# Kernel optimization log

Measured on AMD Instinct MI355X. Metric: run time of the kernel, lower is better.

Reference implementation:

```python
import jax, jax.numpy as jnp
import numpy as np

N = 100000      # nodes
E = 1600000     # edges
D_IN = 128      # input_dim
H = 256         # hidden_dim
L = 3           # num_layers
B = 64          # graphs per batch
BN_EPS = 1e-5


def setup_inputs() -> dict:
    key = jax.random.key(0)
    ks = jax.random.split(key, 8)
    x = jax.random.normal(ks[0], (N, D_IN), dtype=jnp.float32)
    edge_index = jax.random.randint(ks[1], (2, E), 0, N, dtype=jnp.int32)
    batch = jnp.sort(jax.random.randint(ks[2], (N,), 0, B, dtype=jnp.int32))
    W0 = jax.random.normal(ks[3], (D_IN, H), dtype=jnp.float32) / np.sqrt(D_IN)
    W_rest = jax.random.normal(ks[4], (L - 1, H, H), dtype=jnp.float32) / np.sqrt(H)
    b = jax.random.normal(ks[5], (L, H), dtype=jnp.float32) * 0.01
    gamma = 1.0 + jax.random.normal(ks[6], (L, H), dtype=jnp.float32) * 0.01
    beta = jax.random.normal(ks[7], (L, H), dtype=jnp.float32) * 0.01
    return {"x": x, "W0": W0, "W_rest": W_rest, "b": b, "gamma": gamma,
            "beta": beta, "edge_index": edge_index, "batch": batch}


def reference(x, W0, W_rest, b, gamma, beta, edge_index, batch):
    src, dst = edge_index[0], edge_index[1]
    # GCN symmetric normalization with self-loops: deg = in-degree + 1
    deg = jax.ops.segment_sum(jnp.ones((E,), x.dtype), dst, num_segments=N) + 1.0
    dis = jax.lax.rsqrt(deg)                   # deg^{-1/2}, [N]
    enorm = dis[src] * dis[dst]                # per-edge norm, [E]
    self_norm = (dis * dis)[:, None]           # self-loop norm = 1/deg, [N,1]

    def gcn_bn_relu(h, W, bb, g, be):
        h = h @ W                                                  # [N,H]
        agg = jax.ops.segment_sum(h[src] * enorm[:, None], dst, num_segments=N)
        h = agg + h * self_norm + bb                               # self-loop + bias
        # BatchNorm1d (training mode: batch stats, biased variance)
        m = h.mean(axis=0)
        v = h.var(axis=0)
        h = (h - m) * jax.lax.rsqrt(v + BN_EPS) * g + be
        return jax.nn.relu(h)                                      # dropout = identity (eval)

    h = gcn_bn_relu(x, W0, b[0], gamma[0], beta[0])
    for i in range(L - 1):
        h = gcn_bn_relu(h, W_rest[i], b[i + 1], gamma[i + 1], beta[i + 1])

    # segment pooling per graph (att_pool in the original is dead code: not returned)
    counts = jax.ops.segment_sum(jnp.ones((N,), h.dtype), batch, num_segments=B)
    mean_pool = jax.ops.segment_sum(h, batch, num_segments=B) / counts[:, None]
    max_pool = jax.ops.segment_max(h, batch, num_segments=B)
    return jnp.concatenate([mean_pool, max_pool], axis=1)          # [B, 2H]
```

## Files before the change

### kernel.cpp

```cpp
#include <hip/hip_runtime.h>
#include <hip/hip_bf16.h>
#include <stdint.h>


#define NN 100000
#define EE 1600000
#define BB 64
#define MPAD 100096

typedef __attribute__((ext_vector_type(8))) short short8;
typedef __attribute__((ext_vector_type(4))) float f32x4;

__device__ __forceinline__ float bflo(uint32_t v){ return __uint_as_float(v << 16); }
__device__ __forceinline__ float bfhi(uint32_t v){ return __uint_as_float(v & 0xffff0000u); }
__device__ __forceinline__ uint32_t bfrne(float x){
  uint32_t u = __float_as_uint(x);
  return (u + 0x7fffu + ((u >> 16) & 1u)) >> 16;
}
__device__ __forceinline__ uint32_t bfpack(float a, float b){ return bfrne(a) | (bfrne(b) << 16); }

__device__ __forceinline__ void gload_lds16(const void* g, void* l){
  __builtin_amdgcn_global_load_lds(
      (const __attribute__((address_space(1))) uint32_t*)g,
      (__attribute__((address_space(3))) uint32_t*)l, 16, 0, 0);
}

__global__ void k_deg(const int* __restrict__ dst, int* __restrict__ degi){
  for (int e = blockIdx.x * blockDim.x + threadIdx.x; e < EE; e += gridDim.x * blockDim.x)
    atomicAdd(&degi[dst[e]], 1);
}

__global__ void k_dis(const int* __restrict__ degi, float* __restrict__ dis){
  int n = blockIdx.x * 256 + threadIdx.x;
  if (n < NN) dis[n] = rsqrtf((float)degi[n] + 1.0f);
}

__global__ void k_scan1(const int* __restrict__ degi, int* __restrict__ rp, int* __restrict__ bsum){
  __shared__ int lds[256];
  int b = blockIdx.x, t = threadIdx.x;
  int base = b * 1024 + t * 4;
  int v0 = (base + 0 < NN) ? degi[base + 0] : 0;
  int v1 = (base + 1 < NN) ? degi[base + 1] : 0;
  int v2 = (base + 2 < NN) ? degi[base + 2] : 0;
  int v3 = (base + 3 < NN) ? degi[base + 3] : 0;
  int s = v0 + v1 + v2 + v3;
  lds[t] = s; __syncthreads();
  for (int off = 1; off < 256; off <<= 1){
    int x = (t >= off) ? lds[t - off] : 0; __syncthreads();
    lds[t] += x; __syncthreads();
  }
  int excl = lds[t] - s;
  if (t == 255) bsum[b] = lds[255];
  if (base + 0 < NN) rp[base + 0] = excl;
  if (base + 1 < NN) rp[base + 1] = excl + v0;
  if (base + 2 < NN) rp[base + 2] = excl + v0 + v1;
  if (base + 3 < NN) rp[base + 3] = excl + v0 + v1 + v2;
}

__global__ void k_scan2(int* __restrict__ bsum, int nb){
  if (blockIdx.x == 0 && threadIdx.x == 0){
    int run = 0;
    for (int i = 0; i < nb; ++i){ int t = bsum[i]; bsum[i] = run; run += t; }
  }
}

__global__ void k_scan3(int* __restrict__ rp, int* __restrict__ cursor, const int* __restrict__ bsum){
  int b = blockIdx.x, t = threadIdx.x;
  int add = bsum[b];
  int base = b * 1024 + t * 4;
  #pragma unroll
  for (int j = 0; j < 4; ++j){
    int i = base + j;
    if (i < NN){ int v = rp[i] + add; rp[i] = v; cursor[i] = v; }
  }
  if (b == 0 && t == 0) rp[NN] = EE;
}

__global__ void k_fill(const int* __restrict__ src, const int* __restrict__ dst,
                       const float* __restrict__ dis, int* __restrict__ cursor,
                       long long* __restrict__ cp){
  for (int e = blockIdx.x * blockDim.x + threadIdx.x; e < EE; e += gridDim.x * blockDim.x){
    int s = src[e], d = dst[e];
    int pos = atomicAdd(&cursor[d], 1);
    float nrm = dis[s] * dis[d];
    long long v = (long long)(unsigned int)s | ((long long)(unsigned int)__float_as_uint(nrm) << 32);
    cp[pos] = v;
  }
}

__global__ void k_wt(const float* __restrict__ W, uint16_t* __restrict__ Wt, int K){
  int i = blockIdx.x * 256 + threadIdx.x;
  if (i >= 256 * K) return;
  int c = i / K, k = i - c * K;
  Wt[i] = (uint16_t)bfrne(W[k * 256 + c]);
}

__global__ void k_cvtx(const float* __restrict__ x, uint32_t* __restrict__ Xb){
  int i = blockIdx.x * 256 + threadIdx.x;
  if (i >= MPAD * 64) return;
  int row = i >> 6;
  uint32_t r = 0u;
  if (row < NN){
    int col = (i & 63) * 2;
    r = bfpack(x[row * 128 + col], x[row * 128 + col + 1]);
  }
  Xb[i] = r;
}

template<int K>
__global__ void k_agg(const uint32_t* __restrict__ Xin, const int* __restrict__ rp,
                      const long long* __restrict__ cp, const float* __restrict__ dis,
                      uint32_t* __restrict__ Xout){
  constexpr int LPR = K / 2;
  constexpr int RPAR = 256 / LPR;
  constexpr int SEQ = 4;
  int lane = threadIdx.x & (LPR - 1);
  int slot = threadIdx.x / LPR;
  int row0 = blockIdx.x * (RPAR * SEQ);
  for (int rr = 0; rr < SEQ; ++rr){
    int row = row0 + rr * RPAR + slot;
    if (row >= MPAD) continue;
    if (row >= NN){ Xout[(size_t)row * LPR + lane] = 0u; continue; }
    int beg = rp[row], end = rp[row + 1];
    float a0 = 0.f, a1 = 0.f;
    int e = beg;
    for (; e + 8 <= end; e += 8){
      long long p[8];
      #pragma unroll
      for (int u = 0; u < 8; ++u) p[u] = cp[e + u];
      uint32_t v[8];
      #pragma unroll
      for (int u = 0; u < 8; ++u) v[u] = Xin[(size_t)(int)p[u] * LPR + lane];
      #pragma unroll
      for (int u = 0; u < 8; ++u){
        float w = __uint_as_float((uint32_t)((unsigned long long)p[u] >> 32));
        a0 += w * bflo(v[u]); a1 += w * bfhi(v[u]);
      }
    }
    for (; e < end; ++e){
      long long p0 = cp[e];
      int s = (int)p0; float w = __uint_as_float((uint32_t)((unsigned long long)p0 >> 32));
      uint32_t v = Xin[(size_t)s * LPR + lane];
      a0 += w * bflo(v); a1 += w * bfhi(v);
    }
    float dv = dis[row]; float sn = dv * dv;
    uint32_t vs = Xin[(size_t)row * LPR + lane];
    a0 += sn * bflo(vs); a1 += sn * bfhi(vs);
    Xout[(size_t)row * LPR + lane] = bfpack(a0, a1);
  }
}

template<int K>
__global__ __launch_bounds__(256) void k_gemm(const uint16_t* __restrict__ A,
                                              const uint16_t* __restrict__ Bt,
                                              uint32_t* __restrict__ Cb,
                                              float* __restrict__ gstat){
  __shared__ __align__(16) uint16_t lA[2][4096];
  __shared__ __align__(16) uint16_t lB[2][4096];
  __shared__ float lstat[256];
  int tid = threadIdx.x;
  int l = tid & 63;
  int bm = blockIdx.x, bn = blockIdx.y;
  lstat[tid] = 0.f;

  f32x4 acc[4][4];
  #pragma unroll
  for (int m = 0; m < 4; ++m)
    #pragma unroll
    for (int n = 0; n < 4; ++n){ f32x4 z = {0.f,0.f,0.f,0.f}; acc[m][n] = z; }

  int w = tid >> 6, wr = w >> 1, wc = w & 1;
  int rbase = wr * 64, cbase = wc * 64;
  int lrow = l & 15, lk8 = l >> 4;

  auto stage = [&](int kt, int buf){
    #pragma unroll
    for (int i = 0; i < 2; ++i){
      int c = i * 256 + tid;
      int k8 = c >> 7, r = c & 127;
      size_t ga = (size_t)(bm * 128 + r) * K + kt * 32 + k8 * 8;
      size_t gb = (size_t)(bn * 128 + r) * K + kt * 32 + k8 * 8;
      gload_lds16((const char*)(A + ga), (char*)&lA[buf][c * 8]);
      gload_lds16((const char*)(Bt + gb), (char*)&lB[buf][c * 8]);
    }
  };

  stage(0, 0);
  __syncthreads();
  constexpr int NT = K / 32;
  for (int kt = 0; kt < NT; ++kt){
    int cur = kt & 1;
    if (kt + 1 < NT) stage(kt + 1, cur ^ 1);
    short8 afr[4], bfr[4];
    #pragma unroll
    for (int m = 0; m < 4; ++m)
      afr[m] = *(const short8*)&lA[cur][(lk8 * 128 + rbase + m * 16 + lrow) * 8];
    #pragma unroll
    for (int n = 0; n < 4; ++n)
      bfr[n] = *(const short8*)&lB[cur][(lk8 * 128 + cbase + n * 16 + lrow) * 8];
    #pragma unroll
    for (int m = 0; m < 4; ++m)
      #pragma unroll
      for (int n = 0; n < 4; ++n)
        acc[m][n] = __builtin_amdgcn_mfma_f32_16x16x32_bf16(afr[m], bfr[n], acc[m][n], 0, 0, 0);
    __syncthreads();
  }

  int grow0 = bm * 128 + rbase + (l >> 4) * 4;
  int gcol0 = bn * 128 + cbase + (l & 15);
  uint16_t* C16 = (uint16_t*)Cb;
  float sa[4] = {0.f,0.f,0.f,0.f}, sb[4] = {0.f,0.f,0.f,0.f};
  #pragma unroll
  for (int m = 0; m < 4; ++m){
    #pragma unroll
    for (int n = 0; n < 4; ++n){
      int col = gcol0 + n * 16;
      int r0 = grow0 + m * 16;
      f32x4 v = acc[m][n];
      #pragma unroll
      for (int q = 0; q < 4; ++q){
        C16[(size_t)(r0 + q) * 256 + col] = (uint16_t)bfrne(v[q]);
        sa[n] += v[q]; sb[n] += v[q] * v[q];
      }
    }
  }
  #pragma unroll
  for (int n = 0; n < 4; ++n){
    int cl = wc * 64 + n * 16 + lrow;
    atomicAdd(&lstat[cl], sa[n]);
    atomicAdd(&lstat[128 + cl], sb[n]);
  }
  __syncthreads();
  float* rep = gstat + (size_t)(bm & 7) * 512;
  if (tid < 128){
    atomicAdd(&rep[bn * 128 + tid], lstat[tid]);
    atomicAdd(&rep[256 + bn * 128 + tid], lstat[128 + tid]);
  }
}

__global__ void k_finalize(const float* __restrict__ stats, const float* __restrict__ gamma,
                           const float* __restrict__ beta, float* __restrict__ ss){
  int c = threadIdx.x;
  float s = 0.f, s2 = 0.f;
  #pragma unroll
  for (int r = 0; r < 8; ++r){
    s  += stats[r * 512 + c];
    s2 += stats[r * 512 + 256 + c];
  }
  float mean = s / (float)NN;
  float var  = s2 / (float)NN - mean * mean;
  float rstd = rsqrtf(var + 1e-5f);
  float sc = gamma[c] * rstd;
  ss[c] = sc;
  ss[256 + c] = beta[c] - mean * sc;
}

__global__ void k_bnapply(const uint4* __restrict__ Y, const float* __restrict__ ss,
                          uint4* __restrict__ X){
  int i = blockIdx.x * 256 + threadIdx.x;
  if (i >= MPAD * 32) return;
  uint4 v = Y[i];
  int c0 = (i & 31) * 8;
  float r0 = fmaxf(bflo(v.x) * ss[c0 + 0] + ss[256 + c0 + 0], 0.f);
  float r1 = fmaxf(bfhi(v.x) * ss[c0 + 1] + ss[256 + c0 + 1], 0.f);
  float r2 = fmaxf(bflo(v.y) * ss[c0 + 2] + ss[256 + c0 + 2], 0.f);
  float r3 = fmaxf(bfhi(v.y) * ss[c0 + 3] + ss[256 + c0 + 3], 0.f);
  float r4 = fmaxf(bflo(v.z) * ss[c0 + 4] + ss[256 + c0 + 4], 0.f);
  float r5 = fmaxf(bfhi(v.z) * ss[c0 + 5] + ss[256 + c0 + 5], 0.f);
  float r6 = fmaxf(bflo(v.w) * ss[c0 + 6] + ss[256 + c0 + 6], 0.f);
  float r7 = fmaxf(bfhi(v.w) * ss[c0 + 7] + ss[256 + c0 + 7], 0.f);
  uint4 o;
  o.x = bfpack(r0, r1); o.y = bfpack(r2, r3);
  o.z = bfpack(r4, r5); o.w = bfpack(r6, r7);
  X[i] = o;
}

__global__ void k_segstart(const int* __restrict__ batch, int* __restrict__ seg){
  int g = threadIdx.x;
  if (g > BB) return;
  if (g == BB){ seg[BB] = NN; return; }
  int lo = 0, hi = NN;
  while (lo < hi){ int mid = (lo + hi) >> 1; if (batch[mid] < g) lo = mid + 1; else hi = mid; }
  seg[g] = lo;
}

__global__ void k_pool(const uint32_t* __restrict__ X, const int* __restrict__ seg,
                       float* __restrict__ out){
  int g = blockIdx.x, t = threadIdx.x;
  int s = seg[g], e = seg[g + 1];
  float sm0 = 0.f, sm1 = 0.f, mx0 = 0.f, mx1 = 0.f;
  #pragma unroll 4
  for (int r = s; r < e; ++r){
    uint32_t v = X[(size_t)r * 128 + t];
    float a = bflo(v), b2 = bfhi(v);
    sm0 += a; sm1 += b2;
    mx0 = fmaxf(mx0, a); mx1 = fmaxf(mx1, b2);
  }
  float inv = 1.0f / (float)(e - s);
  out[g * 512 + 2 * t] = sm0 * inv;
  out[g * 512 + 2 * t + 1] = sm1 * inv;
  out[g * 512 + 256 + 2 * t] = mx0;
  out[g * 512 + 256 + 2 * t + 1] = mx1;
}

extern "C" void kernel_launch(void* const* d_in, const int* in_sizes, int n_in,
                              void* d_out, int out_size, void* d_ws, size_t ws_size,
                              hipStream_t stream){
  const float* x     = (const float*)d_in[0];
  const float* W0    = (const float*)d_in[1];
  const float* Wr    = (const float*)d_in[2];
  const float* gamma = (const float*)d_in[4];
  const float* beta  = (const float*)d_in[5];
  const int*   ei    = (const int*)d_in[6];
  const int*   batch = (const int*)d_in[7];
  const int* esrc = ei;
  const int* edst = ei + EE;
  float* out = (float*)d_out;

  char* base = (char*)d_ws;
  size_t off = 0;
  auto alloc = [&](size_t b)->char*{
    char* p = base + off; off = (off + b + 255) & ~(size_t)255; return p;
  };
  uint32_t* Xbuf = (uint32_t*)alloc((size_t)MPAD * 256 * 2);
  uint32_t* Xagg = (uint32_t*)alloc((size_t)MPAD * 256 * 2);
  uint32_t* Y    = (uint32_t*)alloc((size_t)MPAD * 256 * 2);
  uint16_t* Wt0  = (uint16_t*)alloc(256 * 128 * 2);
  uint16_t* Wt1  = (uint16_t*)alloc(256 * 256 * 2);
  uint16_t* Wt2  = (uint16_t*)alloc(256 * 256 * 2);
  int*   degi   = (int*)  alloc((size_t)NN * 4);
  float* dis    = (float*)alloc((size_t)NN * 4);
  int*   rp     = (int*)  alloc((size_t)(NN + 1) * 4);
  int*   cursor = (int*)  alloc((size_t)NN * 4);
  int*   bsum   = (int*)  alloc(128 * 4);
  long long* cp = (long long*)alloc((size_t)EE * 8);
  float* stats  = (float*)alloc(8 * 512 * 4);
  float* ss     = (float*)alloc(512 * 4);
  int*   seg    = (int*)  alloc((BB + 1) * 4);

  hipMemsetAsync(degi, 0, (size_t)NN * 4, stream);
  k_deg<<<2048, 256, 0, stream>>>(edst, degi);
  k_dis<<<391, 256, 0, stream>>>(degi, dis);
  k_scan1<<<98, 256, 0, stream>>>(degi, rp, bsum);
  k_scan2<<<1, 1, 0, stream>>>(bsum, 98);
  k_scan3<<<98, 256, 0, stream>>>(rp, cursor, bsum);
  k_fill<<<2048, 256, 0, stream>>>(esrc, edst, dis, cursor, cp);
  k_wt<<<128, 256, 0, stream>>>(W0, Wt0, 128);
  k_wt<<<256, 256, 0, stream>>>(Wr, Wt1, 256);
  k_wt<<<256, 256, 0, stream>>>(Wr + 256 * 256, Wt2, 256);
  k_cvtx<<<MPAD * 64 / 256, 256, 0, stream>>>(x, Xbuf);

  hipMemsetAsync(stats, 0, 8 * 512 * 4, stream);
  k_agg<128><<<MPAD / 16, 256, 0, stream>>>(Xbuf, rp, cp, dis, Xagg);
  k_gemm<128><<<dim3(MPAD / 128, 2), 256, 0, stream>>>((const uint16_t*)Xagg, Wt0, Y, stats);
  k_finalize<<<1, 256, 0, stream>>>(stats, gamma + 0, beta + 0, ss);
  k_bnapply<<<MPAD * 32 / 256, 256, 0, stream>>>((const uint4*)Y, ss, (uint4*)Xbuf);

  hipMemsetAsync(stats, 0, 8 * 512 * 4, stream);
  k_agg<256><<<MPAD / 8, 256, 0, stream>>>(Xbuf, rp, cp, dis, Xagg);
  k_gemm<256><<<dim3(MPAD / 128, 2), 256, 0, stream>>>((const uint16_t*)Xagg, Wt1, Y, stats);
  k_finalize<<<1, 256, 0, stream>>>(stats, gamma + 256, beta + 256, ss);
  k_bnapply<<<MPAD * 32 / 256, 256, 0, stream>>>((const uint4*)Y, ss, (uint4*)Xbuf);

  hipMemsetAsync(stats, 0, 8 * 512 * 4, stream);
  k_agg<256><<<MPAD / 8, 256, 0, stream>>>(Xbuf, rp, cp, dis, Xagg);
  k_gemm<256><<<dim3(MPAD / 128, 2), 256, 0, stream>>>((const uint16_t*)Xagg, Wt2, Y, stats);
  k_finalize<<<1, 256, 0, stream>>>(stats, gamma + 512, beta + 512, ss);
  k_bnapply<<<MPAD * 32 / 256, 256, 0, stream>>>((const uint4*)Y, ss, (uint4*)Xbuf);

  k_segstart<<<1, 128, 0, stream>>>(batch, seg);
  k_pool<<<BB, 128, 0, stream>>>(Xbuf, seg, out);
}
```

Measured before the change: 919.3 us.

## Widen aggregation loads, enlarge GEMM tiles, split pooling, and fuse small setup kernels

After: 770.2 us. -16.2%, faster.

```diff
diff --git a/kernel.cpp b/kernel.cpp
--- a/kernel.cpp
+++ b/kernel.cpp
@@ -18,6 +18,9 @@
   return (u + 0x7fffu + ((u >> 16) & 1u)) >> 16;
 }
 __device__ __forceinline__ uint32_t bfpack(float a, float b){ return bfrne(a) | (bfrne(b) << 16); }
+__device__ __forceinline__ float phi(long long p){
+  return __uint_as_float((uint32_t)((unsigned long long)p >> 32));
+}
 
 __device__ __forceinline__ void gload_lds16(const void* g, void* l){
   __builtin_amdgcn_global_load_lds(
@@ -30,12 +33,8 @@
     atomicAdd(&degi[dst[e]], 1);
 }
 
-__global__ void k_dis(const int* __restrict__ degi, float* __restrict__ dis){
-  int n = blockIdx.x * 256 + threadIdx.x;
-  if (n < NN) dis[n] = rsqrtf((float)degi[n] + 1.0f);
-}
-
-__global__ void k_scan1(const int* __restrict__ degi, int* __restrict__ rp, int* __restrict__ bsum){
+__global__ void k_scan1(const int* __restrict__ degi, int* __restrict__ rp, int* __restrict__ bsum,
+                        float* __restrict__ dis){
   __shared__ int lds[256];
   int b = blockIdx.x, t = threadIdx.x;
   int base = b * 1024 + t * 4;
@@ -43,6 +42,10 @@
   int v1 = (base + 1 < NN) ? degi[base + 1] : 0;
   int v2 = (base + 2 < NN) ? degi[base + 2] : 0;
   int v3 = (base + 3 < NN) ? degi[base + 3] : 0;
+  if (base + 0 < NN) dis[base + 0] = rsqrtf((float)v0 + 1.0f);
+  if (base + 1 < NN) dis[base + 1] = rsqrtf((float)v1 + 1.0f);
+  if (base + 2 < NN) dis[base + 2] = rsqrtf((float)v2 + 1.0f);
+  if (base + 3 < NN) dis[base + 3] = rsqrtf((float)v3 + 1.0f);
   int s = v0 + v1 + v2 + v3;
   lds[t] = s; __syncthreads();
   for (int off = 1; off < 256; off <<= 1){
@@ -88,11 +91,20 @@
   }
 }
 
-__global__ void k_wt(const float* __restrict__ W, uint16_t* __restrict__ Wt, int K){
+__global__ void k_wtall(const float* __restrict__ W0, const float* __restrict__ Wr,
+                        uint16_t* __restrict__ Wt0, uint16_t* __restrict__ Wt1,
+                        uint16_t* __restrict__ Wt2){
   int i = blockIdx.x * 256 + threadIdx.x;
-  if (i >= 256 * K) return;
-  int c = i / K, k = i - c * K;
-  Wt[i] = (uint16_t)bfrne(W[k * 256 + c]);
+  if (i < 32768){
+    int c = i >> 7, k = i & 127;
+    Wt0[i] = (uint16_t)bfrne(W0[k * 256 + c]);
+  } else if (i < 32768 + 131072){
+    int j = i - 32768;
+    int m = j >> 16, jj = j & 65535;
+    int c = jj >> 8, k = jj & 255;
+    uint16_t v = (uint16_t)bfrne(Wr[m * 65536 + k * 256 + c]);
+    if (m == 0) Wt1[jj] = v; else Wt2[jj] = v;
+  }
 }
 
 __global__ void k_cvtx(const float* __restrict__ x, uint32_t* __restrict__ Xb){
@@ -107,61 +119,113 @@
   Xb[i] = r;
 }
 
-template<int K>
-__global__ void k_agg(const uint32_t* __restrict__ Xin, const int* __restrict__ rp,
-                      const long long* __restrict__ cp, const float* __restrict__ dis,
-                      uint32_t* __restrict__ Xout){
-  constexpr int LPR = K / 2;
-  constexpr int RPAR = 256 / LPR;
-  constexpr int SEQ = 4;
-  int lane = threadIdx.x & (LPR - 1);
-  int slot = threadIdx.x / LPR;
-  int row0 = blockIdx.x * (RPAR * SEQ);
-  for (int rr = 0; rr < SEQ; ++rr){
-    int row = row0 + rr * RPAR + slot;
-    if (row >= MPAD) continue;
-    if (row >= NN){ Xout[(size_t)row * LPR + lane] = 0u; continue; }
+__global__ void k_agg256(const uint2* __restrict__ Xin, const int* __restrict__ rp,
+                         const long long* __restrict__ cp, const float* __restrict__ dis,
+                         uint2* __restrict__ Xout){
+  int lane = threadIdx.x & 63;
+  int slot = threadIdx.x >> 6;
+  int row0 = blockIdx.x * 16 + slot;
+  for (int rr = 0; rr < 4; ++rr){
+    int row = row0 + rr * 4;
+    if (row >= NN){
+      if (row < MPAD){ uint2 z = {0u, 0u}; Xout[(size_t)row * 64 + lane] = z; }
+      continue;
+    }
     int beg = rp[row], end = rp[row + 1];
-    float a0 = 0.f, a1 = 0.f;
+    float a0 = 0.f, a1 = 0.f, a2 = 0.f, a3 = 0.f;
     int e = beg;
     for (; e + 8 <= end; e += 8){
-      long long p[8];
+      long long p[8]; uint2 v[8];
       #pragma unroll
       for (int u = 0; u < 8; ++u) p[u] = cp[e + u];
-      uint32_t v[8];
-      #pragma unroll
-      for (int u = 0; u < 8; ++u) v[u] = Xin[(size_t)(int)p[u] * LPR + lane];
+      #pragma unroll
+      for (int u = 0; u < 8; ++u) v[u] = Xin[(size_t)(int)p[u] * 64 + lane];
       #pragma unroll
       for (int u = 0; u < 8; ++u){
-        float w = __uint_as_float((uint32_t)((unsigned long long)p[u] >> 32));
-        a0 += w * bflo(v[u]); a1 += w * bfhi(v[u]);
+        float w = phi(p[u]);
+        a0 += w * bflo(v[u].x); a1 += w * bfhi(v[u].x);
+        a2 += w * bflo(v[u].y); a3 += w * bfhi(v[u].y);
       }
     }
     for (; e < end; ++e){
       long long p0 = cp[e];
-      int s = (int)p0; float w = __uint_as_float((uint32_t)((unsigned long long)p0 >> 32));
-      uint32_t v = Xin[(size_t)s * LPR + lane];
-      a0 += w * bflo(v); a1 += w * bfhi(v);
+      float w = phi(p0);
+      uint2 v = Xin[(size_t)(int)p0 * 64 + lane];
+      a0 += w * bflo(v.x); a1 += w * bfhi(v.x);
+      a2 += w * bflo(v.y); a3 += w * bfhi(v.y);
     }
     float dv = dis[row]; float sn = dv * dv;
-    uint32_t vs = Xin[(size_t)row * LPR + lane];
-    a0 += sn * bflo(vs); a1 += sn * bfhi(vs);
-    Xout[(size_t)row * LPR + lane] = bfpack(a0, a1);
+    uint2 vs = Xin[(size_t)row * 64 + lane];
+    a0 += sn * bflo(vs.x); a1 += sn * bfhi(vs.x);
+    a2 += sn * bflo(vs.y); a3 += sn * bfhi(vs.y);
+    uint2 o; o.x = bfpack(a0, a1); o.y = bfpack(a2, a3);
+    Xout[(size_t)row * 64 + lane] = o;
+  }
+}
+
+__global__ void k_agg128(const uint2* __restrict__ Xin, const int* __restrict__ rp,
+                         const long long* __restrict__ cp, const float* __restrict__ dis,
+                         uint2* __restrict__ Xout){
+  int lane = threadIdx.x & 63;
+  int half = lane >> 5, j = lane & 31;
+  int slot = threadIdx.x >> 6;
+  int row0 = blockIdx.x * 16 + slot;
+  for (int rr = 0; rr < 4; ++rr){
+    int row = row0 + rr * 4;
+    if (row >= NN){
+      if (row < MPAD && half == 0){ uint2 z = {0u, 0u}; Xout[(size_t)row * 32 + j] = z; }
+      continue;
+    }
+    int beg = rp[row], end = rp[row + 1];
+    float a0 = 0.f, a1 = 0.f, a2 = 0.f, a3 = 0.f;
+    int e = beg;
+    for (; e + 8 <= end; e += 8){
+      long long p[4]; uint2 v[4];
+      #pragma unroll
+      for (int u = 0; u < 4; ++u) p[u] = cp[e + u * 2 + half];
+      #pragma unroll
+      for (int u = 0; u < 4; ++u) v[u] = Xin[(size_t)(int)p[u] * 32 + j];
+      #pragma unroll
+      for (int u = 0; u < 4; ++u){
+        float w = phi(p[u]);
+        a0 += w * bflo(v[u].x); a1 += w * bfhi(v[u].x);
+        a2 += w * bflo(v[u].y); a3 += w * bfhi(v[u].y);
+      }
+    }
+    for (; e < end; e += 2){
+      int idx = e + half;
+      bool ok = idx < end;
+      long long p0 = cp[ok ? idx : end - 1];
+      float w = ok ? phi(p0) : 0.f;
+      uint2 v = Xin[(size_t)(int)p0 * 32 + j];
+      a0 += w * bflo(v.x); a1 += w * bfhi(v.x);
+      a2 += w * bflo(v.y); a3 += w * bfhi(v.y);
+    }
+    a0 += __shfl_xor(a0, 32); a1 += __shfl_xor(a1, 32);
+    a2 += __shfl_xor(a2, 32); a3 += __shfl_xor(a3, 32);
+    if (half == 0){
+      float dv = dis[row]; float sn = dv * dv;
+      uint2 vs = Xin[(size_t)row * 32 + j];
+      a0 += sn * bflo(vs.x); a1 += sn * bfhi(vs.x);
+      a2 += sn * bflo(vs.y); a3 += sn * bfhi(vs.y);
+      uint2 o; o.x = bfpack(a0, a1); o.y = bfpack(a2, a3);
+      Xout[(size_t)row * 32 + j] = o;
+    }
   }
 }
 
 template<int K>
-__global__ __launch_bounds__(256) void k_gemm(const uint16_t* __restrict__ A,
+__global__ __launch_bounds__(512) void k_gemm(const uint16_t* __restrict__ A,
                                               const uint16_t* __restrict__ Bt,
                                               uint32_t* __restrict__ Cb,
                                               float* __restrict__ gstat){
-  __shared__ __align__(16) uint16_t lA[2][4096];
+  __shared__ __align__(16) uint16_t lA[2][8192];
   __shared__ __align__(16) uint16_t lB[2][4096];
   __shared__ float lstat[256];
   int tid = threadIdx.x;
   int l = tid & 63;
   int bm = blockIdx.x, bn = blockIdx.y;
-  lstat[tid] = 0.f;
+  if (tid < 256) lstat[tid] = 0.f;
 
   f32x4 acc[4][4];
   #pragma unroll
@@ -176,13 +240,14 @@
   auto stage = [&](int kt, int buf){
     #pragma unroll
     for (int i = 0; i < 2; ++i){
-      int c = i * 256 + tid;
-      int k8 = c >> 7, r = c & 127;
-      size_t ga = (size_t)(bm * 128 + r) * K + kt * 32 + k8 * 8;
-      size_t gb = (size_t)(bn * 128 + r) * K + kt * 32 + k8 * 8;
+      int c = i * 512 + tid;
+      int k8 = c >> 8, r = c & 255;
+      size_t ga = (size_t)(bm * 256 + r) * K + kt * 32 + k8 * 8;
       gload_lds16((const char*)(A + ga), (char*)&lA[buf][c * 8]);
-      gload_lds16((const char*)(Bt + gb), (char*)&lB[buf][c * 8]);
-    }
+    }
+    int k8b = tid >> 7, rb = tid & 127;
+    size_t gb = (size_t)(bn * 128 + rb) * K + kt * 32 + k8b * 8;
+    gload_lds16((const char*)(Bt + gb), (char*)&lB[buf][tid * 8]);
   };
 
   stage(0, 0);
@@ -194,7 +259,7 @@
     short8 afr[4], bfr[4];
     #pragma unroll
     for (int m = 0; m < 4; ++m)
-      afr[m] = *(const short8*)&lA[cur][(lk8 * 128 + rbase + m * 16 + lrow) * 8];
+      afr[m] = *(const short8*)&lA[cur][(lk8 * 256 + rbase + m * 16 + lrow) * 8];
     #pragma unroll
     for (int n = 0; n < 4; ++n)
       bfr[n] = *(const short8*)&lB[cur][(lk8 * 128 + cbase + n * 16 + lrow) * 8];
@@ -206,7 +271,7 @@
     __syncthreads();
   }
 
-  int grow0 = bm * 128 + rbase + (l >> 4) * 4;
+  int grow0 = bm * 256 + rbase + (l >> 4) * 4;
   int gcol0 = bn * 128 + cbase + (l & 15);
   uint16_t* C16 = (uint16_t*)Cb;
   float sa[4] = {0.f,0.f,0.f,0.f}, sb[4] = {0.f,0.f,0.f,0.f};
@@ -226,7 +291,7 @@
   }
   #pragma unroll
   for (int n = 0; n < 4; ++n){
-    int cl = wc * 64 + n * 16 + lrow;
+    int cl = cbase + n * 16 + lrow;
     atomicAdd(&lstat[cl], sa[n]);
     atomicAdd(&lstat[128 + cl], sb[n]);
   }
@@ -238,7 +303,7 @@
   }
 }
 
-__global__ void k_finalize(const float* __restrict__ stats, const float* __restrict__ gamma,
+__global__ void k_finalize(float* __restrict__ stats, const float* __restrict__ gamma,
                            const float* __restrict__ beta, float* __restrict__ ss){
   int c = threadIdx.x;
   float s = 0.f, s2 = 0.f;
@@ -246,6 +311,8 @@
   for (int r = 0; r < 8; ++r){
     s  += stats[r * 512 + c];
     s2 += stats[r * 512 + 256 + c];
+    stats[r * 512 + c] = 0.f;
+    stats[r * 512 + 256 + c] = 0.f;
   }
   float mean = s / (float)NN;
   float var  = s2 / (float)NN - mean * mean;
@@ -284,23 +351,39 @@
   seg[g] = lo;
 }
 
-__global__ void k_pool(const uint32_t* __restrict__ X, const int* __restrict__ seg,
-                       float* __restrict__ out){
-  int g = blockIdx.x, t = threadIdx.x;
+__global__ void k_poolpart(const uint32_t* __restrict__ X, const int* __restrict__ seg,
+                           float* __restrict__ pb){
+  int g = blockIdx.x, c = blockIdx.y, t = threadIdx.x;
   int s = seg[g], e = seg[g + 1];
-  float sm0 = 0.f, sm1 = 0.f, mx0 = 0.f, mx1 = 0.f;
+  int len = e - s;
+  int c0 = s + (int)(((long long)len * c) >> 3);
+  int c1 = s + (int)(((long long)len * (c + 1)) >> 3);
+  float sm0 = 0.f, sm1 = 0.f, mx0 = -1e30f, mx1 = -1e30f;
   #pragma unroll 4
-  for (int r = s; r < e; ++r){
+  for (int r = c0; r < c1; ++r){
     uint32_t v = X[(size_t)r * 128 + t];
     float a = bflo(v), b2 = bfhi(v);
     sm0 += a; sm1 += b2;
     mx0 = fmaxf(mx0, a); mx1 = fmaxf(mx1, b2);
   }
-  float inv = 1.0f / (float)(e - s);
-  out[g * 512 + 2 * t] = sm0 * inv;
-  out[g * 512 + 2 * t + 1] = sm1 * inv;
-  out[g * 512 + 256 + 2 * t] = mx0;
-  out[g * 512 + 256 + 2 * t + 1] = mx1;
+  float* p = pb + (size_t)(g * 8 + c) * 512;
+  p[2 * t] = sm0; p[2 * t + 1] = sm1;
+  p[256 + 2 * t] = mx0; p[256 + 2 * t + 1] = mx1;
+}
+
+__global__ void k_poolred(const float* __restrict__ pb, const int* __restrict__ seg,
+                          float* __restrict__ out){
+  int g = blockIdx.x, cc = threadIdx.x;
+  float s = 0.f, m = -1e30f;
+  #pragma unroll
+  for (int c = 0; c < 8; ++c){
+    const float* p = pb + (size_t)(g * 8 + c) * 512;
+    s += p[cc];
+    m = fmaxf(m, p[256 + cc]);
+  }
+  float inv = 1.0f / (float)(seg[g + 1] - seg[g]);
+  out[g * 512 + cc] = s * inv;
+  out[g * 512 + 256 + cc] = m;
 }
 
 extern "C" void kernel_launch(void* const* d_in, const int* in_sizes, int n_in,
@@ -337,37 +420,34 @@
   float* stats  = (float*)alloc(8 * 512 * 4);
   float* ss     = (float*)alloc(512 * 4);
   int*   seg    = (int*)  alloc((BB + 1) * 4);
+  float* pb     = (float*)alloc((size_t)BB * 8 * 512 * 4);
 
   hipMemsetAsync(degi, 0, (size_t)NN * 4, stream);
+  hipMemsetAsync(stats, 0, 8 * 512 * 4, stream);
   k_deg<<<2048, 256, 0, stream>>>(edst, degi);
-  k_dis<<<391, 256, 0, stream>>>(degi, dis);
-  k_scan1<<<98, 256, 0, stream>>>(degi, rp, bsum);
+  k_scan1<<<98, 256, 0, stream>>>(degi, rp, bsum, dis);
   k_scan2<<<1, 1, 0, stream>>>(bsum, 98);
   k_scan3<<<98, 256, 0, stream>>>(rp, cursor, bsum);
   k_fill<<<2048, 256, 0, stream>>>(esrc, edst, dis, cursor, cp);
-  k_wt<<<128, 256, 0, stream>>>(W0, Wt0, 128);
-  k_wt<<<256, 256, 0, stream>>>(Wr, Wt1, 256);
-  k_wt<<<256, 256, 0, stream>>>(Wr + 256 * 256, Wt2, 256);
+  k_wtall<<<640, 256, 0, stream>>>(W0, Wr, Wt0, Wt1, Wt2);
   k_cvtx<<<MPAD * 64 / 256, 256, 0, stream>>>(x, Xbuf);
 
-  hipMemsetAsync(stats, 0, 8 * 512 * 4, stream);
-  k_agg<128><<<MPAD / 16, 256, 0, stream>>>(Xbuf, rp, cp, dis, Xagg);
-  k_gemm<128><<<dim3(MPAD / 128, 2), 256, 0, stream>>>((const uint16_t*)Xagg, Wt0, Y, stats);
+  k_agg128<<<MPAD / 16, 256, 0, stream>>>((const uint2*)Xbuf, rp, cp, dis, (uint2*)Xagg);
+  k_gemm<128><<<dim3(MPAD / 256, 2), 512, 0, stream>>>((const uint16_t*)Xagg, Wt0, Y, stats);
   k_finalize<<<1, 256, 0, stream>>>(stats, gamma + 0, beta + 0, ss);
   k_bnapply<<<MPAD * 32 / 256, 256, 0, stream>>>((const uint4*)Y, ss, (uint4*)Xbuf);
 
-  hipMemsetAsync(stats, 0, 8 * 512 * 4, stream);
-  k_agg<256><<<MPAD / 8, 256, 0, stream>>>(Xbuf, rp, cp, dis, Xagg);
-  k_gemm<256><<<dim3(MPAD / 128, 2), 256, 0, stream>>>((const uint16_t*)Xagg, Wt1, Y, stats);
+  k_agg256<<<MPAD / 16, 256, 0, stream>>>((const uint2*)Xbuf, rp, cp, dis, (uint2*)Xagg);
+  k_gemm<256><<<dim3(MPAD / 256, 2), 512, 0, stream>>>((const uint16_t*)Xagg, Wt1, Y, stats);
   k_finalize<<<1, 256, 0, stream>>>(stats, gamma + 256, beta + 256, ss);
   k_bnapply<<<MPAD * 32 / 256, 256, 0, stream>>>((const uint4*)Y, ss, (uint4*)Xbuf);
 
-  hipMemsetAsync(stats, 0, 8 * 512 * 4, stream);
-  k_agg<256><<<MPAD / 8, 256, 0, stream>>>(Xbuf, rp, cp, dis, Xagg);
-  k_gemm<256><<<dim3(MPAD / 128, 2), 256, 0, stream>>>((const uint16_t*)Xagg, Wt2, Y, stats);
+  k_agg256<<<MPAD / 16, 256, 0, stream>>>((const uint2*)Xbuf, rp, cp, dis, (uint2*)Xagg);
+  k_gemm<256><<<dim3(MPAD / 256, 2), 512, 0, stream>>>((const uint16_t*)Xagg, Wt2, Y, stats);
   k_finalize<<<1, 256, 0, stream>>>(stats, gamma + 512, beta + 512, ss);
   k_bnapply<<<MPAD * 32 / 256, 256, 0, stream>>>((const uint4*)Y, ss, (uint4*)Xbuf);
 
   k_segstart<<<1, 128, 0, stream>>>(batch, seg);
-  k_pool<<<BB, 128, 0, stream>>>(Xbuf, seg, out);
-}
+  k_poolpart<<<dim3(BB, 8), 128, 0, stream>>>(Xbuf, seg, pb);
+  k_poolred<<<BB, 256, 0, stream>>>(pb, seg, out);
+}
```
